# Kernel tuning notes

Hardware: AMD Instinct MI355X
Metric: run time of the kernel (lower is better)

Reference implementation:

```python
import jax, jax.numpy as jnp
import numpy as np

NEG = -1.0e9  # neg_inf_val from the torch module
B, L, H, M = 512, 512, 256, 24


def setup_inputs() -> dict:
    key = jax.random.key(0)
    k1, k2, k3 = jax.random.split(key, 3)
    word_encodings = jax.random.normal(k1, (B, L, H), jnp.float32)
    # word lengths in [M, L]; num_morphemes constant = M (so padded-morpheme
    # selection is a static reshape, matching torch's masked_select output)
    word_lengths = jax.random.randint(k2, (B,), M, L + 1).astype(jnp.int32)
    num_morphemes = jnp.full((B,), M, jnp.int32)
    W = jax.random.normal(k3, (H, 1), jnp.float32) * 0.05
    b = jnp.zeros((1,), jnp.float32)
    return {"word_encodings": word_encodings, "word_lengths": word_lengths,
            "num_morphemes": num_morphemes, "W": W, "b": b}


def _best_paths(scores, word_lengths, num_morphemes, mask3d):
    # top-(M) separator positions, +1 so index 0 is a dump slot
    sep_idx = jax.lax.top_k(scores, M)[1] + 1                      # [B, M]
    idx_mask = jnp.arange(M)[None, :] >= (num_morphemes - 1)[:, None]
    sep_idx = jnp.where(idx_mask, 0, sep_idx)
    onehot = jnp.zeros((B, L + 1), jnp.int32)
    onehot = onehot.at[jnp.arange(B)[:, None], sep_idx].set(1)
    onehot = jnp.roll(onehot[:, 1:], 1, axis=1)                    # [B, L]
    char2morph = jnp.cumsum(onehot, axis=1)                        # [B, L]
    bpm = jax.nn.one_hot(char2morph, M, dtype=jnp.int32)           # [B, L, M]
    bpm = jnp.where(mask3d, 0, bpm)
    return bpm.astype(bool)


def _marginals(scores, word_lengths, num_morphemes, mask3d):
    log_sig = jax.nn.log_sigmoid(scores)          # [B, L]
    log_1ms = jax.nn.log_sigmoid(-scores)         # [B, L]
    beta_prior = jnp.full((B, L, M), NEG, jnp.float32)
    beta_prior = beta_prior.at[jnp.arange(B), word_lengths - 1,
                               num_morphemes - 1].set(0.0)
    pad = jnp.full((B, 1), NEG, jnp.float32)

    # alpha forward scan over chars
    alpha0 = jnp.full((B, M), NEG, jnp.float32).at[:, 0].set(0.0)
    def a_step(prev, xs):
        ls, l1 = xs                                # each [B]
        stay = prev + l1[:, None]
        shift = jnp.concatenate([pad, prev[:, :-1]], axis=1) + ls[:, None]
        new = jnp.logaddexp(stay, shift)
        return new, new
    _, alpha_rest = jax.lax.scan(a_step, alpha0,
                                 (log_sig[:, :L - 1].T, log_1ms[:, :L - 1].T))
    alpha = jnp.concatenate([alpha0[None], alpha_rest], axis=0)    # [L, B, M]
    alpha = alpha.transpose(1, 0, 2)                               # [B, L, M]

    # beta backward scan
    beta_init = jnp.full((B, M), NEG, jnp.float32)
    def b_step(nxt, xs):
        ls, l1, bp = xs                            # [B],[B],[B,M]
        stay = nxt + l1[:, None]
        shift = jnp.concatenate([nxt[:, 1:], pad], axis=1) + ls[:, None]
        bt = jnp.logaddexp(jnp.logaddexp(stay, shift), bp)
        return bt, bt
    _, beta = jax.lax.scan(b_step, beta_init,
                           (log_sig.T, log_1ms.T, beta_prior.transpose(1, 0, 2)),
                           reverse=True)
    beta = beta.transpose(1, 0, 2)                                 # [B, L, M]

    z = alpha[jnp.arange(B), word_lengths - 1, num_morphemes - 1]
    marg = jnp.exp(alpha + beta - z[:, None, None])
    return jnp.where(mask3d, 0.0, marg)


def reference(word_encodings, word_lengths, num_morphemes, W, b):
    pos = jnp.arange(L)
    scores = (word_encodings @ W)[..., 0] + b[0]                   # [B, L]
    score_mask = pos[None, :] >= (word_lengths - 1)[:, None]
    scores = jnp.where(score_mask, NEG, scores)

    mask3d = (pos[None, :, None] >= word_lengths[:, None, None]) | \
             (jnp.arange(M)[None, None, :] >= num_morphemes[:, None, None])

    bpm = _best_paths(scores, word_lengths, num_morphemes, mask3d)
    marg = _marginals(scores, word_lengths, num_morphemes, mask3d)

    menc = jnp.einsum('blh,blm->bmh', word_encodings, marg)
    res_scores = jnp.where(bpm, marg - 1.0, marg)
    residuals = jax.lax.stop_gradient(
        jnp.einsum('blh,blm->bmh', word_encodings, res_scores))
    menc = (menc - residuals).reshape(B * M, H)
    return menc, bpm
```

## Files before the change

kernel.cpp:

```cpp
#include <hip/hip_runtime.h>

namespace {
constexpr int BATCH = 512;
constexpr int SEQL  = 512;
constexpr int HID   = 256;
constexpr int MORPH = 24;
constexpr float NEGV = -1.0e9f;
constexpr int NTHR  = 1024;
constexpr int NWAVE = 16;
}

extern "C" __global__ __launch_bounds__(1024)
void morphseg_kernel(const float* __restrict__ we,
                     const int*   __restrict__ wlen,
                     const int*   __restrict__ nmorph,
                     const float* __restrict__ Wv,
                     const float* __restrict__ bias,
                     float* __restrict__ out)
{
    const int b    = blockIdx.x;
    const int tid  = threadIdx.x;
    const int lane = tid & 63;
    const int wave = tid >> 6;

    __shared__ unsigned s_keys[SEQL];
    __shared__ int s_hist[256];
    __shared__ int s_c2m[SEQL];
    __shared__ float s_acc[MORPH][HID];
    __shared__ unsigned long long s_eqm[8];
    __shared__ unsigned long long s_ind[8];
    __shared__ unsigned s_p, s_T;
    __shared__ int s_Kr, s_KrF, s_done;

    const int wl = wlen[b];
    const int nm = nmorph[b];
    const int K  = nm - 1;
    const float b0 = bias[0];
    const float* __restrict__ werow = we + (size_t)b * (SEQL * HID);

    auto okey = [](float f) -> unsigned {
        unsigned u = __float_as_uint(f);
        return u ^ (unsigned)(((int)u >> 31) | 0x80000000);
    };
    const unsigned KEYNEG = okey(NEGV);

    if (tid < SEQL) s_keys[tid] = KEYNEG;
    {
        float* af = &s_acc[0][0];
        for (int i = tid; i < MORPH * HID; i += NTHR) af[i] = 0.0f;
    }
    if (tid == 0) { s_p = 0u; s_Kr = K; s_done = 0; }
    __syncthreads();

    const float4 w4 = reinterpret_cast<const float4*>(Wv)[lane];
    const int nvalid = wl - 1;
    for (int l = wave; l < nvalid; l += NWAVE) {
        const float4 v = reinterpret_cast<const float4*>(werow + (size_t)l * HID)[lane];
        float p = v.x * w4.x + v.y * w4.y + v.z * w4.z + v.w * w4.w;
        #pragma unroll
        for (int off = 32; off >= 1; off >>= 1)
            p += __shfl_xor(p, off, 64);
        if (lane == 0) s_keys[l] = okey(p + b0);
    }
    __syncthreads();

    int done = 0;
    for (int pass = 0; pass < 4 && !done; ++pass) {
        const int shift = 24 - 8 * pass;
        if (tid < 256) s_hist[tid] = 0;
        __syncthreads();
        if (tid < SEQL) {
            const unsigned k = s_keys[tid];
            const bool act = (pass == 0) ||
                             ((k >> (shift + 8)) == (s_p >> (shift + 8)));
            if (act) atomicAdd(&s_hist[(k >> shift) & 255], 1);
        }
        __syncthreads();
        if (wave == 0) {
            const int v0 = lane * 4;
            const int h0 = s_hist[v0], h1 = s_hist[v0 + 1];
            const int h2 = s_hist[v0 + 2], h3 = s_hist[v0 + 3];
            const int local = h0 + h1 + h2 + h3;
            int T = local;
            #pragma unroll
            for (int off = 1; off < 64; off <<= 1) {
                const int u = __shfl_down(T, off, 64);
                if (lane + off < 64) T += u;
            }
            const int A  = T - local;
            const int S3 = A + h3, S2 = S3 + h2, S1 = S2 + h1, S0 = S1 + h0;
            const int Kr = s_Kr;
            const unsigned p = s_p;
            int v = -1, Sv = 0, Sv1 = 0;
            if (A  < Kr && Kr <= S3) { v = v0 + 3; Sv = S3; Sv1 = A;  }
            if (S3 < Kr && Kr <= S2) { v = v0 + 2; Sv = S2; Sv1 = S3; }
            if (S2 < Kr && Kr <= S1) { v = v0 + 1; Sv = S1; Sv1 = S2; }
            if (S1 < Kr && Kr <= S0) { v = v0 + 0; Sv = S0; Sv1 = S1; }
            if (v >= 0) {
                const unsigned pv = p | ((unsigned)v << shift);
                if (Sv == Kr) {
                    s_T = pv - 1u; s_KrF = 0; s_done = 1;
                } else if (shift == 0) {
                    s_T = pv; s_KrF = Kr - Sv1; s_done = 1;
                } else {
                    s_p = pv; s_Kr = Kr - Sv1;
                }
            }
        }
        __syncthreads();
        done = s_done;
    }

    const unsigned Tf = s_T;
    const int KrF = s_KrF;
    unsigned k = (tid < SEQL) ? s_keys[tid] : 0u;
    const bool gt = (tid < SEQL) && (k > Tf);
    const bool eq = (tid < SEQL) && (k == Tf);
    const unsigned long long eb = __ballot(eq);
    if (lane == 0 && wave < 8) s_eqm[wave] = eb;
    __syncthreads();
    int f = 0;
    if (tid < SEQL) {
        const unsigned long long lowmask = (1ull << lane) - 1ull;
        int r = 0;
        #pragma unroll
        for (int q = 0; q < 8; ++q) {
            const unsigned long long w = s_eqm[q];
            r += (q < wave) ? __popcll(w) : ((q == wave) ? __popcll(w & lowmask) : 0);
        }
        f = gt || (eq && r < KrF);
    }
    const unsigned long long fb = __ballot(f);
    if (lane == 0 && wave < 8) s_ind[wave] = fb;
    __syncthreads();
    if (tid < SEQL) {
        const unsigned long long lowmask = (1ull << lane) - 1ull;
        int cnt = 0;
        #pragma unroll
        for (int q = 0; q < 8; ++q) {
            const unsigned long long w = s_ind[q];
            cnt += (q < wave) ? __popcll(w) : ((q == wave) ? __popcll(w & lowmask) : 0);
        }
        s_c2m[tid] = cnt;
    }
    __syncthreads();

    float* __restrict__ bpm = out + (size_t)BATCH * MORPH * HID + (size_t)b * (SEQL * MORPH);
    for (int v = tid; v < SEQL * MORPH / 4; v += NTHR) {
        const int l  = v / 6;
        const int q  = v - l * 6;
        const int c  = s_c2m[l];
        const int mb = q * 4;
        const bool valid = (l < wl);
        float4 o;
        o.x = (valid && c == mb + 0 && mb + 0 < nm) ? 1.0f : 0.0f;
        o.y = (valid && c == mb + 1 && mb + 1 < nm) ? 1.0f : 0.0f;
        o.z = (valid && c == mb + 2 && mb + 2 < nm) ? 1.0f : 0.0f;
        o.w = (valid && c == mb + 3 && mb + 3 < nm) ? 1.0f : 0.0f;
        reinterpret_cast<float4*>(bpm)[v] = o;
    }

    {
        const int start = (wave * wl) / NWAVE;
        const int end   = ((wave + 1) * wl) / NWAVE;
        float4 acc = {0.f, 0.f, 0.f, 0.f};
        int mcur = -1;
        for (int l = start; l < end; ++l) {
            const int mm = s_c2m[l];
            if (mm != mcur) {
                if (mcur >= 0) {
                    atomicAdd(&s_acc[mcur][lane * 4 + 0], acc.x);
                    atomicAdd(&s_acc[mcur][lane * 4 + 1], acc.y);
                    atomicAdd(&s_acc[mcur][lane * 4 + 2], acc.z);
                    atomicAdd(&s_acc[mcur][lane * 4 + 3], acc.w);
                    acc.x = acc.y = acc.z = acc.w = 0.f;
                }
                mcur = mm;
            }
            const float4 v = reinterpret_cast<const float4*>(werow + (size_t)l * HID)[lane];
            acc.x += v.x; acc.y += v.y; acc.z += v.z; acc.w += v.w;
        }
        if (mcur >= 0) {
            atomicAdd(&s_acc[mcur][lane * 4 + 0], acc.x);
            atomicAdd(&s_acc[mcur][lane * 4 + 1], acc.y);
            atomicAdd(&s_acc[mcur][lane * 4 + 2], acc.z);
            atomicAdd(&s_acc[mcur][lane * 4 + 3], acc.w);
        }
    }
    __syncthreads();

    float* __restrict__ mout = out + (size_t)b * (MORPH * HID);
    {
        const float4* af = reinterpret_cast<const float4*>(&s_acc[0][0]);
        for (int i = tid; i < MORPH * HID / 4; i += NTHR)
            reinterpret_cast<float4*>(mout)[i] = af[i];
    }
}

extern "C" void kernel_launch(void* const* d_in, const int* in_sizes, int n_in,
                              void* d_out, int out_size, void* d_ws, size_t ws_size,
                              hipStream_t stream) {
    const float* we     = (const float*)d_in[0];
    const int*   wlen   = (const int*)d_in[1];
    const int*   nmorph = (const int*)d_in[2];
    const float* Wv     = (const float*)d_in[3];
    const float* bias   = (const float*)d_in[4];
    float* out = (float*)d_out;
    morphseg_kernel<<<dim3(BATCH), dim3(NTHR), 0, stream>>>(we, wlen, nmorph, Wv, bias, out);
}
```

Baseline: 64.63 us.

## Split fused kernel into score, select, and segment-sum kernels with finer blocks

Splits the single per-batch 1024-thread kernel into three launches. The first computes scores into a workspace using 8 blocks per batch row. The second does the radix top-k selection and writes the best-path output. The third does the segment sums over 64-row chunks, again 8 blocks per batch row, and uses global atomics only for morphemes that straddle a chunk boundary. The aim is more parallelism and better occupancy than one large block per batch, at the cost of two extra launches, workspace traffic, and reading the encodings twice from global memory.

Result: slower. 129.6 us (+100.5%).

```diff
diff --git a/kernel.cpp b/kernel.cpp
--- a/kernel.cpp
+++ b/kernel.cpp
@@ -6,62 +6,70 @@
 constexpr int HID   = 256;
 constexpr int MORPH = 24;
 constexpr float NEGV = -1.0e9f;
-constexpr int NTHR  = 1024;
-constexpr int NWAVE = 16;
-}
-
-extern "C" __global__ __launch_bounds__(1024)
-void morphseg_kernel(const float* __restrict__ we,
-                     const int*   __restrict__ wlen,
-                     const int*   __restrict__ nmorph,
-                     const float* __restrict__ Wv,
-                     const float* __restrict__ bias,
-                     float* __restrict__ out)
+}
+
+__device__ __forceinline__ unsigned okey(float f) {
+    unsigned u = __float_as_uint(f);
+    return u ^ (unsigned)(((int)u >> 31) | 0x80000000);
+}
+
+extern "C" __global__ __launch_bounds__(256)
+void k_scores(const float* __restrict__ we, const int* __restrict__ wlen,
+              const float* __restrict__ Wv, const float* __restrict__ bias,
+              unsigned* __restrict__ keys, float* __restrict__ menc)
 {
-    const int b    = blockIdx.x;
-    const int tid  = threadIdx.x;
-    const int lane = tid & 63;
-    const int wave = tid >> 6;
+    const int blk = blockIdx.x;
+    const int b = blk >> 3, q = blk & 7;
+    const int tid = threadIdx.x, lane = tid & 63, wave = tid >> 6;
+    const int wl = wlen[b];
+    const float b0 = bias[0];
+    const float* __restrict__ werow = we + (size_t)b * (SEQL * HID);
+    const unsigned KEYNEG = okey(NEGV);
+
+    {
+        const float4 z = {0.f, 0.f, 0.f, 0.f};
+        float4* mz = reinterpret_cast<float4*>(menc) + (size_t)blk * 192;
+        if (tid < 192) mz[tid] = z;
+    }
+
+    const float4 w4 = reinterpret_cast<const float4*>(Wv)[lane];
+    const int rs = q * 64;
+    const int nvalid = wl - 1;
+    for (int l = rs + wave; l < rs + 64; l += 4) {
+        unsigned kk = KEYNEG;
+        if (l < nvalid) {
+            const float4 v = reinterpret_cast<const float4*>(werow + (size_t)l * HID)[lane];
+            float p = v.x * w4.x + v.y * w4.y + v.z * w4.z + v.w * w4.w;
+            #pragma unroll
+            for (int off = 32; off >= 1; off >>= 1)
+                p += __shfl_xor(p, off, 64);
+            kk = okey(p + b0);
+        }
+        if (lane == 0) keys[b * SEQL + l] = kk;
+    }
+}
+
+extern "C" __global__ __launch_bounds__(512)
+void k_select(const unsigned* __restrict__ keys, const int* __restrict__ wlen,
+              const int* __restrict__ nmorph, unsigned char* __restrict__ c2m_g,
+              float* __restrict__ out)
+{
+    const int b = blockIdx.x;
+    const int tid = threadIdx.x, lane = tid & 63, wave = tid >> 6;
 
     __shared__ unsigned s_keys[SEQL];
     __shared__ int s_hist[256];
     __shared__ int s_c2m[SEQL];
-    __shared__ float s_acc[MORPH][HID];
-    __shared__ unsigned long long s_eqm[8];
-    __shared__ unsigned long long s_ind[8];
+    __shared__ unsigned long long s_eqm[8], s_ind[8];
     __shared__ unsigned s_p, s_T;
     __shared__ int s_Kr, s_KrF, s_done;
 
     const int wl = wlen[b];
     const int nm = nmorph[b];
     const int K  = nm - 1;
-    const float b0 = bias[0];
-    const float* __restrict__ werow = we + (size_t)b * (SEQL * HID);
-
-    auto okey = [](float f) -> unsigned {
-        unsigned u = __float_as_uint(f);
-        return u ^ (unsigned)(((int)u >> 31) | 0x80000000);
-    };
-    const unsigned KEYNEG = okey(NEGV);
-
-    if (tid < SEQL) s_keys[tid] = KEYNEG;
-    {
-        float* af = &s_acc[0][0];
-        for (int i = tid; i < MORPH * HID; i += NTHR) af[i] = 0.0f;
-    }
+
+    s_keys[tid] = keys[b * SEQL + tid];
     if (tid == 0) { s_p = 0u; s_Kr = K; s_done = 0; }
-    __syncthreads();
-
-    const float4 w4 = reinterpret_cast<const float4*>(Wv)[lane];
-    const int nvalid = wl - 1;
-    for (int l = wave; l < nvalid; l += NWAVE) {
-        const float4 v = reinterpret_cast<const float4*>(werow + (size_t)l * HID)[lane];
-        float p = v.x * w4.x + v.y * w4.y + v.z * w4.z + v.w * w4.w;
-        #pragma unroll
-        for (int off = 32; off >= 1; off >>= 1)
-            p += __shfl_xor(p, off, 64);
-        if (lane == 0) s_keys[l] = okey(p + b0);
-    }
     __syncthreads();
 
     int done = 0;
@@ -69,7 +77,7 @@
         const int shift = 24 - 8 * pass;
         if (tid < 256) s_hist[tid] = 0;
         __syncthreads();
-        if (tid < SEQL) {
+        {
             const unsigned k = s_keys[tid];
             const bool act = (pass == 0) ||
                              ((k >> (shift + 8)) == (s_p >> (shift + 8)));
@@ -98,13 +106,9 @@
             if (S1 < Kr && Kr <= S0) { v = v0 + 0; Sv = S0; Sv1 = S1; }
             if (v >= 0) {
                 const unsigned pv = p | ((unsigned)v << shift);
-                if (Sv == Kr) {
-                    s_T = pv - 1u; s_KrF = 0; s_done = 1;
-                } else if (shift == 0) {
-                    s_T = pv; s_KrF = Kr - Sv1; s_done = 1;
-                } else {
-                    s_p = pv; s_Kr = Kr - Sv1;
-                }
+                if (Sv == Kr)       { s_T = pv - 1u; s_KrF = 0;        s_done = 1; }
+                else if (shift == 0){ s_T = pv;      s_KrF = Kr - Sv1; s_done = 1; }
+                else                { s_p = pv;      s_Kr = Kr - Sv1; }
             }
         }
         __syncthreads();
@@ -113,44 +117,45 @@
 
     const unsigned Tf = s_T;
     const int KrF = s_KrF;
-    unsigned k = (tid < SEQL) ? s_keys[tid] : 0u;
-    const bool gt = (tid < SEQL) && (k > Tf);
-    const bool eq = (tid < SEQL) && (k == Tf);
+    const unsigned k = s_keys[tid];
+    const bool gt = (k > Tf);
+    const bool eq = (k == Tf);
     const unsigned long long eb = __ballot(eq);
-    if (lane == 0 && wave < 8) s_eqm[wave] = eb;
-    __syncthreads();
-    int f = 0;
-    if (tid < SEQL) {
+    if (lane == 0) s_eqm[wave] = eb;
+    __syncthreads();
+    int f;
+    {
         const unsigned long long lowmask = (1ull << lane) - 1ull;
         int r = 0;
         #pragma unroll
-        for (int q = 0; q < 8; ++q) {
-            const unsigned long long w = s_eqm[q];
-            r += (q < wave) ? __popcll(w) : ((q == wave) ? __popcll(w & lowmask) : 0);
+        for (int qq = 0; qq < 8; ++qq) {
+            const unsigned long long w = s_eqm[qq];
+            r += (qq < wave) ? __popcll(w) : ((qq == wave) ? __popcll(w & lowmask) : 0);
         }
         f = gt || (eq && r < KrF);
     }
     const unsigned long long fb = __ballot(f);
-    if (lane == 0 && wave < 8) s_ind[wave] = fb;
-    __syncthreads();
-    if (tid < SEQL) {
+    if (lane == 0) s_ind[wave] = fb;
+    __syncthreads();
+    {
         const unsigned long long lowmask = (1ull << lane) - 1ull;
         int cnt = 0;
         #pragma unroll
-        for (int q = 0; q < 8; ++q) {
-            const unsigned long long w = s_ind[q];
-            cnt += (q < wave) ? __popcll(w) : ((q == wave) ? __popcll(w & lowmask) : 0);
+        for (int qq = 0; qq < 8; ++qq) {
+            const unsigned long long w = s_ind[qq];
+            cnt += (qq < wave) ? __popcll(w) : ((qq == wave) ? __popcll(w & lowmask) : 0);
         }
         s_c2m[tid] = cnt;
+        c2m_g[b * SEQL + tid] = (unsigned char)cnt;
     }
     __syncthreads();
 
     float* __restrict__ bpm = out + (size_t)BATCH * MORPH * HID + (size_t)b * (SEQL * MORPH);
-    for (int v = tid; v < SEQL * MORPH / 4; v += NTHR) {
+    for (int v = tid; v < SEQL * MORPH / 4; v += 512) {
         const int l  = v / 6;
-        const int q  = v - l * 6;
+        const int qv = v - l * 6;
         const int c  = s_c2m[l];
-        const int mb = q * 4;
+        const int mb = qv * 4;
         const bool valid = (l < wl);
         float4 o;
         o.x = (valid && c == mb + 0 && mb + 0 < nm) ? 1.0f : 0.0f;
@@ -159,41 +164,75 @@
         o.w = (valid && c == mb + 3 && mb + 3 < nm) ? 1.0f : 0.0f;
         reinterpret_cast<float4*>(bpm)[v] = o;
     }
-
-    {
-        const int start = (wave * wl) / NWAVE;
-        const int end   = ((wave + 1) * wl) / NWAVE;
-        float4 acc = {0.f, 0.f, 0.f, 0.f};
-        int mcur = -1;
-        for (int l = start; l < end; ++l) {
-            const int mm = s_c2m[l];
-            if (mm != mcur) {
-                if (mcur >= 0) {
-                    atomicAdd(&s_acc[mcur][lane * 4 + 0], acc.x);
-                    atomicAdd(&s_acc[mcur][lane * 4 + 1], acc.y);
-                    atomicAdd(&s_acc[mcur][lane * 4 + 2], acc.z);
-                    atomicAdd(&s_acc[mcur][lane * 4 + 3], acc.w);
-                    acc.x = acc.y = acc.z = acc.w = 0.f;
-                }
-                mcur = mm;
+}
+
+extern "C" __global__ __launch_bounds__(256)
+void k_menc(const float* __restrict__ we, const int* __restrict__ wlen,
+            const unsigned char* __restrict__ c2m_g, float* __restrict__ menc)
+{
+    const int blk = blockIdx.x;
+    const int b = blk >> 3, q = blk & 7;
+    const int tid = threadIdx.x, lane = tid & 63, wave = tid >> 6;
+    const int wl = wlen[b];
+    const int rs = q * 64;
+    if (rs >= wl) return;
+    const int re = min(rs + 64, wl);
+
+    __shared__ float s_acc[MORPH][HID];
+    __shared__ unsigned char s_cl[66];
+
+    if (tid < 66) {
+        const int row = rs - 1 + tid;
+        s_cl[tid] = (row >= 0 && row < SEQL) ? c2m_g[b * SEQL + row] : (unsigned char)255;
+    }
+    {
+        float* af = &s_acc[0][0];
+        for (int i = tid; i < MORPH * HID; i += 256) af[i] = 0.0f;
+    }
+    __syncthreads();
+
+    const int m_first = s_cl[1];
+    const int m_last  = s_cl[re - rs];
+
+    const int n  = re - rs;
+    const int lw0 = rs + (wave * n) / 4;
+    const int lw1 = rs + ((wave + 1) * n) / 4;
+    const float* __restrict__ werow = we + (size_t)b * (SEQL * HID);
+
+    float4 acc = {0.f, 0.f, 0.f, 0.f};
+    int mcur = -1;
+    for (int l = lw0; l < lw1; ++l) {
+        const int mm = s_cl[l - rs + 1];
+        if (mm != mcur) {
+            if (mcur >= 0) {
+                atomicAdd(&s_acc[mcur][lane * 4 + 0], acc.x);
+                atomicAdd(&s_acc[mcur][lane * 4 + 1], acc.y);
+                atomicAdd(&s_acc[mcur][lane * 4 + 2], acc.z);
+                atomicAdd(&s_acc[mcur][lane * 4 + 3], acc.w);
+                acc.x = acc.y = acc.z = acc.w = 0.f;
             }
-            const float4 v = reinterpret_cast<const float4*>(werow + (size_t)l * HID)[lane];
-            acc.x += v.x; acc.y += v.y; acc.z += v.z; acc.w += v.w;
-        }
-        if (mcur >= 0) {
-            atomicAdd(&s_acc[mcur][lane * 4 + 0], acc.x);
-            atomicAdd(&s_acc[mcur][lane * 4 + 1], acc.y);
-            atomicAdd(&s_acc[mcur][lane * 4 + 2], acc.z);
-            atomicAdd(&s_acc[mcur][lane * 4 + 3], acc.w);
-        }
-    }
-    __syncthreads();
-
-    float* __restrict__ mout = out + (size_t)b * (MORPH * HID);
-    {
-        const float4* af = reinterpret_cast<const float4*>(&s_acc[0][0]);
-        for (int i = tid; i < MORPH * HID / 4; i += NTHR)
-            reinterpret_cast<float4*>(mout)[i] = af[i];
+            mcur = mm;
+        }
+        const float4 v = reinterpret_cast<const float4*>(werow + (size_t)l * HID)[lane];
+        acc.x += v.x; acc.y += v.y; acc.z += v.z; acc.w += v.w;
+    }
+    if (mcur >= 0) {
+        atomicAdd(&s_acc[mcur][lane * 4 + 0], acc.x);
+        atomicAdd(&s_acc[mcur][lane * 4 + 1], acc.y);
+        atomicAdd(&s_acc[mcur][lane * 4 + 2], acc.z);
+        atomicAdd(&s_acc[mcur][lane * 4 + 3], acc.w);
+    }
+    __syncthreads();
+
+    const bool sp = (q > 0) && ((int)s_cl[0] == m_first);
+    const bool sn = (re < wl) && ((int)s_cl[65] == m_last);
+
+    float* __restrict__ mout = menc + (size_t)b * (MORPH * HID);
+    for (int m = m_first; m <= m_last; ++m) {
+        const float v = s_acc[m][tid];
+        const bool shared = (m == m_first && sp) || (m == m_last && sn);
+        if (shared) atomicAdd(&mout[m * HID + tid], v);
+        else        mout[m * HID + tid] = v;
     }
 }
 
@@ -206,5 +245,11 @@
     const float* Wv     = (const float*)d_in[3];
     const float* bias   = (const float*)d_in[4];
     float* out = (float*)d_out;
-    morphseg_kernel<<<dim3(BATCH), dim3(NTHR), 0, stream>>>(we, wlen, nmorph, Wv, bias, out);
-}
+
+    unsigned*      keys = (unsigned*)d_ws;
+    unsigned char* c2m  = (unsigned char*)d_ws + (1u << 20);
+
+    k_scores<<<dim3(BATCH * 8), dim3(256), 0, stream>>>(we, wlen, Wv, bias, keys, out);
+    k_select<<<dim3(BATCH), dim3(512), 0, stream>>>(keys, wlen, nmorph, c2m, out);
+    k_menc  <<<dim3(BATCH * 8), dim3(256), 0, stream>>>(we, wlen, c2m, out);
+}
```

## Specialize waves for bpm writes vs segment sums and widen score dot-products

Applied to the files above, without the earlier changes.

Score computation now has each 16-lane group handle a whole row with 16 loads per lane, so one wave covers four rows at a time and the shuffle reduction is shorter. After computing char2morph, waves 12-15 write the best-path mask while waves 0-11 do the segment-sum accumulation, so the two phases can run concurrently instead of back to back. Output writes use nontemporal stores, and launch bounds now request 8 waves per SIMD (one 1024-thread block per CU). The trade-off is fewer waves streaming the word encodings during the sum phase, which may lengthen that critical path.

Measured after the change: 64.25 us. About the same (-0.6%).

```diff
diff --git a/kernel.cpp b/kernel.cpp
--- a/kernel.cpp
+++ b/kernel.cpp
@@ -7,10 +7,16 @@
 constexpr int MORPH = 24;
 constexpr float NEGV = -1.0e9f;
 constexpr int NTHR  = 1024;
-constexpr int NWAVE = 16;
-}
-
-extern "C" __global__ __launch_bounds__(1024)
+}
+
+typedef float f4v __attribute__((ext_vector_type(4)));
+
+__device__ __forceinline__ unsigned okey(float f) {
+    unsigned u = __float_as_uint(f);
+    return u ^ (unsigned)(((int)u >> 31) | 0x80000000);
+}
+
+extern "C" __global__ __launch_bounds__(NTHR, 8)
 void morphseg_kernel(const float* __restrict__ we,
                      const int*   __restrict__ wlen,
                      const int*   __restrict__ nmorph,
@@ -27,8 +33,7 @@
     __shared__ int s_hist[256];
     __shared__ int s_c2m[SEQL];
     __shared__ float s_acc[MORPH][HID];
-    __shared__ unsigned long long s_eqm[8];
-    __shared__ unsigned long long s_ind[8];
+    __shared__ unsigned long long s_eqm[8], s_ind[8];
     __shared__ unsigned s_p, s_T;
     __shared__ int s_Kr, s_KrF, s_done;
 
@@ -37,11 +42,6 @@
     const int K  = nm - 1;
     const float b0 = bias[0];
     const float* __restrict__ werow = we + (size_t)b * (SEQL * HID);
-
-    auto okey = [](float f) -> unsigned {
-        unsigned u = __float_as_uint(f);
-        return u ^ (unsigned)(((int)u >> 31) | 0x80000000);
-    };
     const unsigned KEYNEG = okey(NEGV);
 
     if (tid < SEQL) s_keys[tid] = KEYNEG;
@@ -52,15 +52,34 @@
     if (tid == 0) { s_p = 0u; s_Kr = K; s_done = 0; }
     __syncthreads();
 
-    const float4 w4 = reinterpret_cast<const float4*>(Wv)[lane];
-    const int nvalid = wl - 1;
-    for (int l = wave; l < nvalid; l += NWAVE) {
-        const float4 v = reinterpret_cast<const float4*>(werow + (size_t)l * HID)[lane];
-        float p = v.x * w4.x + v.y * w4.y + v.z * w4.z + v.w * w4.w;
-        #pragma unroll
-        for (int off = 32; off >= 1; off >>= 1)
-            p += __shfl_xor(p, off, 64);
-        if (lane == 0) s_keys[l] = okey(p + b0);
+    {
+        const int hg = lane & 15;
+        const int rg = lane >> 4;
+        const float4* __restrict__ W4 = reinterpret_cast<const float4*>(Wv);
+        const float4 w0 = W4[hg * 4 + 0], w1 = W4[hg * 4 + 1];
+        const float4 w2 = W4[hg * 4 + 2], w3 = W4[hg * 4 + 3];
+        const int nvalid = wl - 1;
+        for (int l0 = wave * 4; l0 < nvalid; l0 += 64) {
+            const int row = l0 + rg;
+            if (row < nvalid) {
+                const float4* __restrict__ rp =
+                    reinterpret_cast<const float4*>(werow + (size_t)row * HID);
+                const float4 v0 = rp[hg * 4 + 0], v1 = rp[hg * 4 + 1];
+                const float4 v2 = rp[hg * 4 + 2], v3 = rp[hg * 4 + 3];
+                float d = v0.x * w0.x; d = fmaf(v0.y, w0.y, d);
+                d = fmaf(v0.z, w0.z, d); d = fmaf(v0.w, w0.w, d);
+                d = fmaf(v1.x, w1.x, d); d = fmaf(v1.y, w1.y, d);
+                d = fmaf(v1.z, w1.z, d); d = fmaf(v1.w, w1.w, d);
+                d = fmaf(v2.x, w2.x, d); d = fmaf(v2.y, w2.y, d);
+                d = fmaf(v2.z, w2.z, d); d = fmaf(v2.w, w2.w, d);
+                d = fmaf(v3.x, w3.x, d); d = fmaf(v3.y, w3.y, d);
+                d = fmaf(v3.z, w3.z, d); d = fmaf(v3.w, w3.w, d);
+                #pragma unroll
+                for (int off = 1; off < 16; off <<= 1)
+                    d += __shfl_xor(d, off, 64);
+                if (hg == 0) s_keys[row] = okey(d + b0);
+            }
+        }
     }
     __syncthreads();
 
@@ -71,9 +90,8 @@
         __syncthreads();
         if (tid < SEQL) {
             const unsigned k = s_keys[tid];
-            const bool act = (pass == 0) ||
-                             ((k >> (shift + 8)) == (s_p >> (shift + 8)));
-            if (act) atomicAdd(&s_hist[(k >> shift) & 255], 1);
+            if (pass == 0 || (k >> (shift + 8)) == (s_p >> (shift + 8)))
+                atomicAdd(&s_hist[(k >> shift) & 255], 1);
         }
         __syncthreads();
         if (wave == 0) {
@@ -98,13 +116,9 @@
             if (S1 < Kr && Kr <= S0) { v = v0 + 0; Sv = S0; Sv1 = S1; }
             if (v >= 0) {
                 const unsigned pv = p | ((unsigned)v << shift);
-                if (Sv == Kr) {
-                    s_T = pv - 1u; s_KrF = 0; s_done = 1;
-                } else if (shift == 0) {
-                    s_T = pv; s_KrF = Kr - Sv1; s_done = 1;
-                } else {
-                    s_p = pv; s_Kr = Kr - Sv1;
-                }
+                if (Sv == Kr)        { s_T = pv - 1u; s_KrF = 0;        s_done = 1; }
+                else if (shift == 0) { s_T = pv;      s_KrF = Kr - Sv1; s_done = 1; }
+                else                 { s_p = pv;      s_Kr = Kr - Sv1; }
             }
         }
         __syncthreads();
@@ -113,56 +127,52 @@
 
     const unsigned Tf = s_T;
     const int KrF = s_KrF;
-    unsigned k = (tid < SEQL) ? s_keys[tid] : 0u;
+    const unsigned k = (tid < SEQL) ? s_keys[tid] : 0u;
     const bool gt = (tid < SEQL) && (k > Tf);
     const bool eq = (tid < SEQL) && (k == Tf);
     const unsigned long long eb = __ballot(eq);
     if (lane == 0 && wave < 8) s_eqm[wave] = eb;
     __syncthreads();
-    int f = 0;
-    if (tid < SEQL) {
-        const unsigned long long lowmask = (1ull << lane) - 1ull;
+
+    auto prefix8 = [&](const unsigned long long* w8, int pos) -> int {
+        const int wi = pos >> 6;
+        const unsigned long long lowmask = (1ull << (pos & 63)) - 1ull;
         int r = 0;
         #pragma unroll
-        for (int q = 0; q < 8; ++q) {
-            const unsigned long long w = s_eqm[q];
-            r += (q < wave) ? __popcll(w) : ((q == wave) ? __popcll(w & lowmask) : 0);
-        }
-        f = gt || (eq && r < KrF);
-    }
+        for (int q2 = 0; q2 < 8; ++q2) {
+            const unsigned long long w = w8[q2];
+            r += (q2 < wi) ? __popcll(w) : ((q2 == wi) ? __popcll(w & lowmask) : 0);
+        }
+        return r;
+    };
+
+    int f = 0;
+    if (tid < SEQL) f = gt || (eq && prefix8(s_eqm, tid) < KrF);
     const unsigned long long fb = __ballot(f);
     if (lane == 0 && wave < 8) s_ind[wave] = fb;
     __syncthreads();
-    if (tid < SEQL) {
-        const unsigned long long lowmask = (1ull << lane) - 1ull;
-        int cnt = 0;
-        #pragma unroll
-        for (int q = 0; q < 8; ++q) {
-            const unsigned long long w = s_ind[q];
-            cnt += (q < wave) ? __popcll(w) : ((q == wave) ? __popcll(w & lowmask) : 0);
-        }
-        s_c2m[tid] = cnt;
-    }
-    __syncthreads();
-
-    float* __restrict__ bpm = out + (size_t)BATCH * MORPH * HID + (size_t)b * (SEQL * MORPH);
-    for (int v = tid; v < SEQL * MORPH / 4; v += NTHR) {
-        const int l  = v / 6;
-        const int q  = v - l * 6;
-        const int c  = s_c2m[l];
-        const int mb = q * 4;
-        const bool valid = (l < wl);
-        float4 o;
-        o.x = (valid && c == mb + 0 && mb + 0 < nm) ? 1.0f : 0.0f;
-        o.y = (valid && c == mb + 1 && mb + 1 < nm) ? 1.0f : 0.0f;
-        o.z = (valid && c == mb + 2 && mb + 2 < nm) ? 1.0f : 0.0f;
-        o.w = (valid && c == mb + 3 && mb + 3 < nm) ? 1.0f : 0.0f;
-        reinterpret_cast<float4*>(bpm)[v] = o;
-    }
-
-    {
-        const int start = (wave * wl) / NWAVE;
-        const int end   = ((wave + 1) * wl) / NWAVE;
+    if (tid < SEQL) s_c2m[tid] = prefix8(s_ind, tid);
+    __syncthreads();
+
+    if (wave >= 12) {
+        const int sub = tid - 768;
+        float* __restrict__ bpm = out + (size_t)BATCH * MORPH * HID + (size_t)b * (SEQL * MORPH);
+        for (int v = sub; v < SEQL * MORPH / 4; v += 256) {
+            const int l  = v / 6;
+            const int qv = v - l * 6;
+            const int c  = s_c2m[l];
+            const int mb = qv * 4;
+            const bool valid = (l < wl);
+            f4v o;
+            o.x = (valid && c == mb + 0 && mb + 0 < nm) ? 1.0f : 0.0f;
+            o.y = (valid && c == mb + 1 && mb + 1 < nm) ? 1.0f : 0.0f;
+            o.z = (valid && c == mb + 2 && mb + 2 < nm) ? 1.0f : 0.0f;
+            o.w = (valid && c == mb + 3 && mb + 3 < nm) ? 1.0f : 0.0f;
+            __builtin_nontemporal_store(o, reinterpret_cast<f4v*>(bpm) + v);
+        }
+    } else {
+        const int start = (wave * wl) / 12;
+        const int end   = ((wave + 1) * wl) / 12;
         float4 acc = {0.f, 0.f, 0.f, 0.f};
         int mcur = -1;
         for (int l = start; l < end; ++l) {
@@ -189,11 +199,11 @@
     }
     __syncthreads();
 
-    float* __restrict__ mout = out + (size_t)b * (MORPH * HID);
     {
-        const float4* af = reinterpret_cast<const float4*>(&s_acc[0][0]);
+        float* __restrict__ mout = out + (size_t)b * (MORPH * HID);
+        const f4v* af = reinterpret_cast<const f4v*>(&s_acc[0][0]);
         for (int i = tid; i < MORPH * HID / 4; i += NTHR)
-            reinterpret_cast<float4*>(mout)[i] = af[i];
+            __builtin_nontemporal_store(af[i], reinterpret_cast<f4v*>(mout) + i);
     }
 }
 
```
